# Kernel tuning notes

Measured on AMD Instinct MI355X. Metric: run time of the kernel, lower is better.

## Reference

```python
import jax, jax.numpy as jnp
import numpy as np

N, E, M, A, D = 100000, 3200000, 4096, 32, 16
G, V1, V2, O1 = 10, 20, 10, 20


def _lin(key, fin, fout, scale=0.1):
    kw, kb = jax.random.split(key)
    W = jax.random.normal(kw, (fin, fout), jnp.float32) * scale
    b = jax.random.normal(kb, (fout,), jnp.float32) * scale
    return W, b


def setup_inputs():
    key = jax.random.key(0)
    ks = jax.random.split(key, 32)
    inp = {}
    inp["x1"] = jax.random.normal(ks[0], (N, 15), jnp.float32)
    inp["x2"] = jax.random.normal(ks[1], (4,), jnp.float32)
    inp["edges"] = jax.random.randint(ks[2], (2, E), 0, N)
    inp["attack_src"] = jax.random.randint(ks[3], (M, A), 0, N)
    inp["attack_dst"] = jax.random.randint(ks[4], (M, A), 0, N)
    inp["attack_armies"] = jax.random.uniform(ks[5], (M, A), jnp.float32, 1.0, 20.0)
    inp["deploy_target"] = jax.random.randint(ks[6], (M, D), 0, N)
    inp["deploy_armies"] = jax.random.uniform(ks[7], (M, D), jnp.float32, 1.0, 10.0)
    inp["init_W"], inp["init_b"] = _lin(ks[8], 15, G)
    for i, fin in zip((1, 2, 3), (G + 15, 2 * G + 15, 3 * G + 15)):
        k1, k2, k3, k4 = jax.random.split(ks[8 + i], 4)
        inp[f"g{i}_Wl"] = jax.random.normal(k1, (fin, G), jnp.float32) * 0.1
        inp[f"g{i}_Wr"] = jax.random.normal(k2, (fin, G), jnp.float32) * 0.1
        inp[f"g{i}_att"] = jax.random.normal(k3, (G,), jnp.float32) * 0.1
        inp[f"g{i}_b"] = jax.random.normal(k4, (G,), jnp.float32) * 0.1
    inp["vt_W"], inp["vt_b"] = _lin(ks[12], 15 + G + 4, V1)
    inp["va_W"], inp["va_b"] = _lin(ks[13], V1, 1)
    inp["vv_W"], inp["vv_b"] = _lin(ks[14], V1, V2)
    inp["vl_W"], inp["vl_b"] = _lin(ks[15], V2, 1)
    inp["at_W"], inp["at_b"] = _lin(ks[16], 48, O1)
    inp["dt_W"], inp["dt_b"] = _lin(ks[17], 23, O1)
    inp["oa_W"], inp["oa_b"] = _lin(ks[18], O1, 1)
    inp["ov_W"], inp["ov_b"] = _lin(ks[19], O1, 1)
    return inp


def _gatv2(x, src, dst, Wl, Wr, att, bias, n):
    # GATv2 (PyG defaults: heads=1, negative_slope=0.2); dropout omitted (eval mode)
    xl = x @ Wl  # source-side transform  [N, G]
    xr = x @ Wr  # target-side transform  [N, G]
    e = jax.nn.leaky_relu(xl[src] + xr[dst], 0.2) @ att  # [Etot]
    emax = jax.ops.segment_max(e, dst, num_segments=n)
    ex = jnp.exp(e - emax[dst])
    denom = jax.ops.segment_sum(ex, dst, num_segments=n)
    alpha = ex / denom[dst]  # edge softmax per target node
    return jax.ops.segment_sum(alpha[:, None] * xl[src], dst, num_segments=n) + bias


def _forward(x1, x2, edges, attack_src, attack_dst, attack_armies,
             deploy_target, deploy_armies, p):
    n = x1.shape[0]
    loop = jnp.arange(n)
    src = jnp.concatenate([edges[0], loop])  # add_self_loops (PyG default)
    dst = jnp.concatenate([edges[1], loop])
    x_ = jax.nn.relu(x1 @ p["init_W"] + p["init_b"])  # Dropout = identity in eval
    xa = jax.nn.relu(_gatv2(jnp.concatenate([x_, x1], 1), src, dst,
                            p["g1_Wl"], p["g1_Wr"], p["g1_att"], p["g1_b"], n))
    xb = jax.nn.relu(_gatv2(jnp.concatenate([xa, x_, x1], 1), src, dst,
                            p["g2_Wl"], p["g2_Wr"], p["g2_att"], p["g2_b"], n))
    xc = jax.nn.relu(_gatv2(jnp.concatenate([xb, xa, x_, x1], 1), src, dst,
                            p["g3_Wl"], p["g3_Wr"], p["g3_att"], p["g3_b"], n))
    # per-move order features, batched over all moves at once: [M,A,*] / [M,D,*]
    x1d = x1[attack_dst]  # [M, A, 15]
    extra = 0.6 * attack_armies - 0.7 * (x1d[..., 3] + x1d[..., 4])
    att_feat = jnp.concatenate([xc[attack_src], xc[attack_dst],
                                x1[attack_src][..., 3:], x1d[..., 1:],
                                attack_armies[..., None], extra[..., None]], -1)  # [M,A,48]
    dep_feat = jnp.concatenate([xc[deploy_target], x1[deploy_target][..., 3:],
                                deploy_armies[..., None]], -1)  # [M,D,23]
    orders = jax.nn.relu(jnp.concatenate(
        [att_feat @ p["at_W"] + p["at_b"], dep_feat @ p["dt_W"] + p["dt_b"]], 1))  # [M,A+D,O1]
    oattn = jax.nn.softmax(orders @ p["oa_W"] + p["oa_b"], axis=1)  # softmax over orders
    pm = jnp.sum(oattn * (orders @ p["ov_W"] + p["ov_b"]), axis=(1, 2))  # [M]
    # value head: attention-pool over nodes
    vfeat = jnp.concatenate([xc, x1, jnp.tile(x2, (n, 1))], 1)  # [N, 29]
    v = jax.nn.relu(vfeat @ p["vt_W"] + p["vt_b"])
    vattn = jax.nn.softmax(v @ p["va_W"] + p["va_b"], axis=0)
    vagg = jax.nn.relu(jnp.sum(vattn * (v @ p["vv_W"] + p["vv_b"]), axis=0))
    V = jnp.tanh(vagg @ p["vl_W"] + p["vl_b"]).reshape(())
    return V, jax.nn.log_softmax(pm)


def reference(x1, x2, edges, attack_src, attack_dst, attack_armies,
              deploy_target, deploy_armies,
              init_W, init_b,
              g1_Wl, g1_Wr, g1_att, g1_b,
              g2_Wl, g2_Wr, g2_att, g2_b,
              g3_Wl, g3_Wr, g3_att, g3_b,
              vt_W, vt_b, va_W, va_b, vv_W, vv_b, vl_W, vl_b,
              at_W, at_b, dt_W, dt_b, oa_W, oa_b, ov_W, ov_b):
    p = dict(init_W=init_W, init_b=init_b,
             g1_Wl=g1_Wl, g1_Wr=g1_Wr, g1_att=g1_att, g1_b=g1_b,
             g2_Wl=g2_Wl, g2_Wr=g2_Wr, g2_att=g2_att, g2_b=g2_b,
             g3_Wl=g3_Wl, g3_Wr=g3_Wr, g3_att=g3_att, g3_b=g3_b,
             vt_W=vt_W, vt_b=vt_b, va_W=va_W, va_b=va_b, vv_W=vv_W, vv_b=vv_b,
             vl_W=vl_W, vl_b=vl_b, at_W=at_W, at_b=at_b, dt_W=dt_W, dt_b=dt_b,
             oa_W=oa_W, oa_b=oa_b, ov_W=ov_W, ov_b=ov_b)
    return _forward(x1, x2, edges, attack_src, attack_dst, attack_armies,
                    deploy_target, deploy_armies, p)
```

## Files before the change

kernel.cpp:

```cpp
#include <hip/hip_runtime.h>
#include <math.h>


#define PAD 12
#define LP 8
#define PFP 16
#define MAXB 784
#define CHK 8192

__device__ __forceinline__ float lrelu02(float v) { return v > 0.f ? v : 0.2f * v; }

__device__ __forceinline__ unsigned pk_bf16(float a, float b)
{
    unsigned ua = __float_as_uint(a), ub = __float_as_uint(b);
    ua += 0x7fffu + ((ua >> 16) & 1u);
    ub += 0x7fffu + ((ub >> 16) & 1u);
    return (ua >> 16) | (ub & 0xffff0000u);
}
__device__ __forceinline__ float bf_lo(unsigned u) { return __uint_as_float(u << 16); }
__device__ __forceinline__ float bf_hi(unsigned u) { return __uint_as_float(u & 0xffff0000u); }

template <int NS>
__device__ __forceinline__ void transform_body(
    int n, const float* __restrict__ s0, const float* __restrict__ s1,
    const float* __restrict__ s2, const float* __restrict__ x1,
    const float* __restrict__ Wl, const float* __restrict__ Wr,
    unsigned* __restrict__ XLb, float* __restrict__ XR)
{
    float al[10], ar[10];
#pragma unroll
    for (int g = 0; g < 10; ++g) { al[g] = 0.f; ar[g] = 0.f; }
    int o = 0;
#define TB_BLOCK(SP)                                                        \
    {                                                                       \
        const float4* pr = (const float4*)((SP) + n * PAD);                 \
        float4 v0 = pr[0], v1 = pr[1], v2 = pr[2];                          \
        float fv[10] = {v0.x, v0.y, v0.z, v0.w, v1.x, v1.y, v1.z, v1.w,     \
                        v2.x, v2.y};                                        \
        _Pragma("unroll") for (int k = 0; k < 10; ++k)                      \
        {                                                                   \
            _Pragma("unroll") for (int g = 0; g < 10; ++g)                  \
            {                                                               \
                al[g] += fv[k] * Wl[(o + k) * 10 + g];                      \
                ar[g] += fv[k] * Wr[(o + k) * 10 + g];                      \
            }                                                               \
        }                                                                   \
        o += 10;                                                            \
    }
    if constexpr (NS >= 1) TB_BLOCK(s0)
    if constexpr (NS >= 2) TB_BLOCK(s1)
    if constexpr (NS >= 3) TB_BLOCK(s2)
#undef TB_BLOCK
#pragma unroll
    for (int k = 0; k < 15; ++k) {
        float fv = x1[n * 15 + k];
#pragma unroll
        for (int g = 0; g < 10; ++g) {
            al[g] += fv * Wl[(o + k) * 10 + g];
            ar[g] += fv * Wr[(o + k) * 10 + g];
        }
    }
    uint4 q0;
    q0.x = pk_bf16(al[0], al[1]);
    q0.y = pk_bf16(al[2], al[3]);
    q0.z = pk_bf16(al[4], al[5]);
    q0.w = pk_bf16(al[6], al[7]);
    uint4 q1;
    q1.x = pk_bf16(al[8], al[9]);
    q1.y = 0; q1.z = 0; q1.w = 0;
    uint4* pb = (uint4*)(XLb + (size_t)n * LP);
    pb[0] = q0;
    pb[1] = q1;
    float4* po = (float4*)(XR + n * PAD);
    po[0] = make_float4(ar[0], ar[1], ar[2], ar[3]);
    po[1] = make_float4(ar[4], ar[5], ar[6], ar[7]);
    po[2] = make_float4(ar[8], ar[9], 0.f, 0.f);
}

__global__ __launch_bounds__(256) void k_a1_init(
    const int* __restrict__ edst, int E, unsigned short* __restrict__ pos,
    int* __restrict__ cntg, int PA,
    const float* __restrict__ x1, const float* __restrict__ W,
    const float* __restrict__ b, float* __restrict__ xo, int N, int NBK)
{
    if ((int)blockIdx.x < PA) {
        __shared__ int h[MAXB];
        for (int j = threadIdx.x; j < NBK; j += 256) h[j] = 0;
        __syncthreads();
        int base = blockIdx.x * CHK;
        for (int k = 0; k < CHK / 256; ++k) {
            int i = base + k * 256 + threadIdx.x;
            if (i < E) {
                int bkt = edst[i] >> 7;
                int p = atomicAdd(&h[bkt], 1);
                pos[i] = (unsigned short)p;
            }
        }
        __syncthreads();
        for (int j = threadIdx.x; j < NBK; j += 256)
            cntg[(size_t)j * PA + blockIdx.x] = h[j];
    } else {
        int n = ((int)blockIdx.x - PA) * 256 + (int)threadIdx.x;
        if (n >= N) return;
        float acc[10];
#pragma unroll
        for (int g = 0; g < 10; ++g) acc[g] = b[g];
#pragma unroll
        for (int k = 0; k < 15; ++k) {
            float fv = x1[n * 15 + k];
#pragma unroll
            for (int g = 0; g < 10; ++g) acc[g] += fv * W[k * 10 + g];
        }
        float4* po = (float4*)(xo + n * PAD);
        po[0] = make_float4(fmaxf(acc[0], 0.f), fmaxf(acc[1], 0.f),
                            fmaxf(acc[2], 0.f), fmaxf(acc[3], 0.f));
        po[1] = make_float4(fmaxf(acc[4], 0.f), fmaxf(acc[5], 0.f),
                            fmaxf(acc[6], 0.f), fmaxf(acc[7], 0.f));
        po[2] = make_float4(fmaxf(acc[8], 0.f), fmaxf(acc[9], 0.f), 0.f, 0.f);
    }
}

__global__ __launch_bounds__(1024) void k_scanA(
    const int* __restrict__ cntg, int* __restrict__ bases,
    int* __restrict__ bsumA, int TOT)
{
    __shared__ int wsum[16];
    int t = threadIdx.x;
    int i = blockIdx.x * 1024 + t;
    int lane = t & 63, w = t >> 6;
    int x = (i < TOT) ? cntg[i] : 0;
    int incl = x;
#pragma unroll
    for (int off = 1; off < 64; off <<= 1) {
        int u = __shfl_up(incl, off);
        if (lane >= off) incl += u;
    }
    if (lane == 63) wsum[w] = incl;
    __syncthreads();
    int woff = 0;
    for (int k = 0; k < w; ++k) woff += wsum[k];
    incl += woff;
    if (i < TOT) bases[i] = incl - x;
    if (t == 1023) bsumA[blockIdx.x] = incl;
}

__global__ __launch_bounds__(512) void k_scanB(
    const int* __restrict__ bsumA, int* __restrict__ boffA, int NBLKA,
    float* __restrict__ vsums, int* __restrict__ rowptr, int N, int Etot)
{
    __shared__ int wsum[8];
    int t = threadIdx.x;
    int lane = t & 63, w = t >> 6;
    int x = (t < NBLKA) ? bsumA[t] : 0;
    int incl = x;
#pragma unroll
    for (int off = 1; off < 64; off <<= 1) {
        int u = __shfl_up(incl, off);
        if (lane >= off) incl += u;
    }
    if (lane == 63) wsum[w] = incl;
    __syncthreads();
    int woff = 0;
    for (int k = 0; k < w; ++k) woff += wsum[k];
    incl += woff;
    if (t < NBLKA) boffA[t] = incl - x;
    if (t < 16) vsums[t] = 0.f;
    if (t == 0) rowptr[N] = Etot;
}

__global__ __launch_bounds__(1024) void k_scanC(
    int* __restrict__ bases, const int* __restrict__ boffA, int TOT)
{
    int i = blockIdx.x * 1024 + threadIdx.x;
    if (i < TOT) bases[i] += boffA[blockIdx.x];
}

__global__ __launch_bounds__(256) void k_a2(
    const int* __restrict__ esrc, const int* __restrict__ edst, int E,
    const int* __restrict__ bases, const unsigned short* __restrict__ pos,
    unsigned* __restrict__ pairs, int PA)
{
    int i = blockIdx.x * 256 + threadIdx.x;
    if (i >= E) return;
    int d = edst[i], s = esrc[i];
    int bkt = d >> 7;
    int blk = i / CHK;
    int dest = bases[(size_t)bkt * PA + blk] + (int)pos[i];
    pairs[dest] = (unsigned)s | ((unsigned)(d & 127) << 17);
}

__global__ __launch_bounds__(256) void k_b_tr1(
    const unsigned* __restrict__ pairs, const int* __restrict__ bases,
    int* __restrict__ rowptr, int* __restrict__ deg, int* __restrict__ sidx,
    int N, int NBK, int PA, int E,
    const float* __restrict__ s0a, const float* __restrict__ x1,
    const float* __restrict__ Wl, const float* __restrict__ Wr,
    unsigned* __restrict__ XLb, float* __restrict__ XR, int NB)
{
    if ((int)blockIdx.x < NBK) {
        __shared__ int cnt[128];
        __shared__ int cur[128];
        __shared__ int wtot;
        int t = threadIdx.x;
        if (t < 128) cnt[t] = 0;
        __syncthreads();
        int b = blockIdx.x;
        int p0 = bases[(size_t)b * PA];
        int p1 = (b + 1 < NBK) ? bases[(size_t)(b + 1) * PA] : E;
        int n0 = b << 7;
        int nn = N - n0; nn = nn < 0 ? 0 : (nn > 128 ? 128 : nn);
        for (int i = p0 + t; i < p1; i += 256) atomicAdd(&cnt[pairs[i] >> 17], 1);
        __syncthreads();
        int x = 0, incl = 0;
        if (t < 128) {
            x = cnt[t] + (t < nn ? 1 : 0);
            incl = x;
            int lane = t & 63;
#pragma unroll
            for (int off = 1; off < 64; off <<= 1) {
                int u = __shfl_up(incl, off);
                if (lane >= off) incl += u;
            }
            if (t == 63) wtot = incl;
        }
        __syncthreads();
        int sb = p0 + (b << 7);
        if (t < 128) {
            if (t >= 64) incl += wtot;
            int st = incl - x;
            if (t < nn) {
                int r = sb + st;
                rowptr[n0 + t] = r;
                deg[n0 + t] = cnt[t] + 1;
                sidx[r] = n0 + t;
                cur[t] = st + 1;
            } else {
                cur[t] = st;
            }
        }
        __syncthreads();
        for (int i = p0 + t; i < p1; i += 256) {
            unsigned w = pairs[i];
            int l = w >> 17, s = w & 0x1FFFF;
            int off = atomicAdd(&cur[l], 1);
            sidx[sb + off] = s;
        }
    } else {
        int n = ((int)blockIdx.x - NBK) * 256 + (int)threadIdx.x;
        if (n >= N) return;
        transform_body<1>(n, s0a, nullptr, nullptr, x1, Wl, Wr, XLb, XR);
    }
}

template <int NS>
__global__ __launch_bounds__(256) void k_transform(
    const float* __restrict__ s0, const float* __restrict__ s1,
    const float* __restrict__ s2, const float* __restrict__ x1,
    const float* __restrict__ Wl, const float* __restrict__ Wr,
    unsigned* __restrict__ XLb, float* __restrict__ XR, int N)
{
    int n = blockIdx.x * blockDim.x + threadIdx.x;
    if (n >= N) return;
    transform_body<NS>(n, s0, s1, s2, x1, Wl, Wr, XLb, XR);
}

__global__ __launch_bounds__(256) void k_gather(
    const int* __restrict__ rowptr, const int* __restrict__ deg,
    const int* __restrict__ sidx,
    const unsigned* __restrict__ XLb, const float* __restrict__ XR,
    const float* __restrict__ att, const float* __restrict__ b,
    float* __restrict__ xo, unsigned* __restrict__ PFb,
    const float* __restrict__ x1, int N)
{
    int node = blockIdx.x * 16 + (threadIdx.x >> 4);
    int l16 = threadIdx.x & 15;
    float acc[10];
#pragma unroll
    for (int g = 0; g < 10; ++g) acc[g] = 0.f;
    float den = 0.f;
    float satt[10];
#pragma unroll
    for (int g = 0; g < 10; ++g) satt[g] = att[g];
    if (node < N) {
        const float4* pr = (const float4*)(XR + node * PAD);
        float4 r0 = pr[0], r1 = pr[1], r2 = pr[2];
        float xr[10] = {r0.x, r0.y, r0.z, r0.w, r1.x, r1.y, r1.z, r1.w, r2.x, r2.y};
        int start = rowptr[node];
        int dgr = deg[node];
        int j = l16;
        while (j + 16 < dgr) {
            int s0 = sidx[start + j];
            int s1 = sidx[start + j + 16];
            const unsigned* pl0 = XLb + (size_t)s0 * LP;
            const unsigned* pl1 = XLb + (size_t)s1 * LP;
            uint4 qa = *(const uint4*)pl0;
            unsigned qa4 = pl0[4];
            uint4 qb = *(const uint4*)pl1;
            unsigned qb4 = pl1[4];
            float xa[10] = {bf_lo(qa.x), bf_hi(qa.x), bf_lo(qa.y), bf_hi(qa.y),
                            bf_lo(qa.z), bf_hi(qa.z), bf_lo(qa.w), bf_hi(qa.w),
                            bf_lo(qa4), bf_hi(qa4)};
            float xb[10] = {bf_lo(qb.x), bf_hi(qb.x), bf_lo(qb.y), bf_hi(qb.y),
                            bf_lo(qb.z), bf_hi(qb.z), bf_lo(qb.w), bf_hi(qb.w),
                            bf_lo(qb4), bf_hi(qb4)};
            float ea = 0.f, eb = 0.f;
#pragma unroll
            for (int g = 0; g < 10; ++g) {
                ea += lrelu02(xa[g] + xr[g]) * satt[g];
                eb += lrelu02(xb[g] + xr[g]) * satt[g];
            }
            float exa = __expf(ea), exb = __expf(eb);
#pragma unroll
            for (int g = 0; g < 10; ++g) acc[g] += exa * xa[g] + exb * xb[g];
            den += exa + exb;
            j += 32;
        }
        if (j < dgr) {
            int s = sidx[start + j];
            const unsigned* pl = XLb + (size_t)s * LP;
            uint4 q = *(const uint4*)pl;
            unsigned q4 = pl[4];
            float xl[10] = {bf_lo(q.x), bf_hi(q.x), bf_lo(q.y), bf_hi(q.y),
                            bf_lo(q.z), bf_hi(q.z), bf_lo(q.w), bf_hi(q.w),
                            bf_lo(q4), bf_hi(q4)};
            float e = 0.f;
#pragma unroll
            for (int g = 0; g < 10; ++g) e += lrelu02(xl[g] + xr[g]) * satt[g];
            float ex = __expf(e);
#pragma unroll
            for (int g = 0; g < 10; ++g) acc[g] += ex * xl[g];
            den += ex;
        }
    }
#pragma unroll
    for (int off = 1; off < 16; off <<= 1) {
        den += __shfl_xor(den, off);
#pragma unroll
        for (int g = 0; g < 10; ++g) acc[g] += __shfl_xor(acc[g], off);
    }
    if (node < N && l16 == 0) {
        float inv = 1.f / den;
        float r[10];
#pragma unroll
        for (int g = 0; g < 10; ++g) r[g] = fmaxf(acc[g] * inv + b[g], 0.f);
        float4* po = (float4*)(xo + node * PAD);
        po[0] = make_float4(r[0], r[1], r[2], r[3]);
        po[1] = make_float4(r[4], r[5], r[6], r[7]);
        po[2] = make_float4(r[8], r[9], 0.f, 0.f);
        if (PFb) {
            float xf[14];
#pragma unroll
            for (int k = 0; k < 14; ++k) xf[k] = x1[node * 15 + 1 + k];
            uint4 q0, q1, q2;
            q0.x = pk_bf16(r[0], r[1]);
            q0.y = pk_bf16(r[2], r[3]);
            q0.z = pk_bf16(r[4], r[5]);
            q0.w = pk_bf16(r[6], r[7]);
            q1.x = pk_bf16(r[8], r[9]);
            q1.y = pk_bf16(xf[0], xf[1]);
            q1.z = pk_bf16(xf[2], xf[3]);
            q1.w = pk_bf16(xf[4], xf[5]);
            q2.x = pk_bf16(xf[6], xf[7]);
            q2.y = pk_bf16(xf[8], xf[9]);
            q2.z = pk_bf16(xf[10], xf[11]);
            q2.w = pk_bf16(xf[12], xf[13]);
            uint4* qp = (uint4*)(PFb + (size_t)node * PFP);
            qp[0] = q0;
            qp[1] = q1;
            qp[2] = q2;
        }
    }
}

__global__ __launch_bounds__(256, 4) void k_scores(
    const unsigned* __restrict__ PFb, const float* __restrict__ xc,
    const float* __restrict__ x1, const float* __restrict__ x2,
    const int* __restrict__ asrc, const int* __restrict__ adst,
    const float* __restrict__ aarm,
    const int* __restrict__ dtgt, const float* __restrict__ darm,
    const float* __restrict__ atW, const float* __restrict__ atb,
    const float* __restrict__ dtW, const float* __restrict__ dtb,
    const float* __restrict__ oaW, const float* __restrict__ oab,
    const float* __restrict__ ovW, const float* __restrict__ ovb,
    const float* __restrict__ vtW, const float* __restrict__ vtb,
    const float* __restrict__ vaW, const float* __restrict__ vab,
    const float* __restrict__ vvW, const float* __restrict__ vvb,
    float* __restrict__ vsums, float2* __restrict__ OS,
    int AB, int DB, int NB, int N, int M)
{
    if ((int)blockIdx.x < AB) {
        int i = blockIdx.x * 256 + threadIdx.x;
        if (i >= M * 32) return;
        int m = i >> 5, a = i & 31;
        int s = asrc[i], d = adst[i];
        float arm = aarm[i];
        const uint4* ps = (const uint4*)(PFb + (size_t)s * PFP);
        const uint4* pd = (const uint4*)(PFb + (size_t)d * PFP);
        uint4 sA = ps[0], sB = ps[1], sC = ps[2];
        uint4 dA = pd[0], dB = pd[1], dC = pd[2];
        float fs[24] = {bf_lo(sA.x), bf_hi(sA.x), bf_lo(sA.y), bf_hi(sA.y),
                        bf_lo(sA.z), bf_hi(sA.z), bf_lo(sA.w), bf_hi(sA.w),
                        bf_lo(sB.x), bf_hi(sB.x), bf_lo(sB.y), bf_hi(sB.y),
                        bf_lo(sB.z), bf_hi(sB.z), bf_lo(sB.w), bf_hi(sB.w),
                        bf_lo(sC.x), bf_hi(sC.x), bf_lo(sC.y), bf_hi(sC.y),
                        bf_lo(sC.z), bf_hi(sC.z), bf_lo(sC.w), bf_hi(sC.w)};
        float fd[24] = {bf_lo(dA.x), bf_hi(dA.x), bf_lo(dA.y), bf_hi(dA.y),
                        bf_lo(dA.z), bf_hi(dA.z), bf_lo(dA.w), bf_hi(dA.w),
                        bf_lo(dB.x), bf_hi(dB.x), bf_lo(dB.y), bf_hi(dB.y),
                        bf_lo(dB.z), bf_hi(dB.z), bf_lo(dB.w), bf_hi(dB.w),
                        bf_lo(dC.x), bf_hi(dC.x), bf_lo(dC.y), bf_hi(dC.y),
                        bf_lo(dC.z), bf_hi(dC.z), bf_lo(dC.w), bf_hi(dC.w)};
        float ord[20];
#pragma unroll
        for (int j = 0; j < 20; ++j) ord[j] = atb[j];
#pragma unroll
        for (int k = 0; k < 10; ++k)
#pragma unroll
            for (int j = 0; j < 20; ++j) ord[j] += fs[k] * atW[k * 20 + j];
#pragma unroll
        for (int k = 0; k < 10; ++k)
#pragma unroll
            for (int j = 0; j < 20; ++j) ord[j] += fd[k] * atW[(10 + k) * 20 + j];
#pragma unroll
        for (int k = 0; k < 12; ++k)
#pragma unroll
            for (int j = 0; j < 20; ++j)
                ord[j] += fs[12 + k] * atW[(20 + k) * 20 + j];
#pragma unroll
        for (int k = 0; k < 14; ++k)
#pragma unroll
            for (int j = 0; j < 20; ++j)
                ord[j] += fd[10 + k] * atW[(32 + k) * 20 + j];
        float extra = 0.6f * arm - 0.7f * (fd[12] + fd[13]);
#pragma unroll
        for (int j = 0; j < 20; ++j)
            ord[j] += arm * atW[46 * 20 + j] + extra * atW[47 * 20 + j];
        float asc = oab[0], vsc = ovb[0];
#pragma unroll
        for (int j = 0; j < 20; ++j) {
            float oj = fmaxf(ord[j], 0.f);
            asc += oj * oaW[j];
            vsc += oj * ovW[j];
        }
        OS[(size_t)m * 48 + a] = make_float2(asc, vsc);
    } else if ((int)blockIdx.x < AB + DB) {
        int i = ((int)blockIdx.x - AB) * 256 + threadIdx.x;
        if (i >= M * 16) return;
        int m = i >> 4, dd = i & 15;
        int tg = dtgt[i];
        float arm = darm[i];
        const uint4* pt = (const uint4*)(PFb + (size_t)tg * PFP);
        uint4 tA = pt[0], tB = pt[1], tC = pt[2];
        float ft[24] = {bf_lo(tA.x), bf_hi(tA.x), bf_lo(tA.y), bf_hi(tA.y),
                        bf_lo(tA.z), bf_hi(tA.z), bf_lo(tA.w), bf_hi(tA.w),
                        bf_lo(tB.x), bf_hi(tB.x), bf_lo(tB.y), bf_hi(tB.y),
                        bf_lo(tB.z), bf_hi(tB.z), bf_lo(tB.w), bf_hi(tB.w),
                        bf_lo(tC.x), bf_hi(tC.x), bf_lo(tC.y), bf_hi(tC.y),
                        bf_lo(tC.z), bf_hi(tC.z), bf_lo(tC.w), bf_hi(tC.w)};
        float ord[20];
#pragma unroll
        for (int j = 0; j < 20; ++j) ord[j] = dtb[j];
#pragma unroll
        for (int k = 0; k < 10; ++k)
#pragma unroll
            for (int j = 0; j < 20; ++j) ord[j] += ft[k] * dtW[k * 20 + j];
#pragma unroll
        for (int k = 0; k < 12; ++k)
#pragma unroll
            for (int j = 0; j < 20; ++j)
                ord[j] += ft[12 + k] * dtW[(10 + k) * 20 + j];
#pragma unroll
        for (int j = 0; j < 20; ++j) ord[j] += arm * dtW[22 * 20 + j];
        float asc = oab[0], vsc = ovb[0];
#pragma unroll
        for (int j = 0; j < 20; ++j) {
            float oj = fmaxf(ord[j], 0.f);
            asc += oj * oaW[j];
            vsc += oj * ovW[j];
        }
        OS[(size_t)m * 48 + 32 + dd] = make_float2(asc, vsc);
    } else {
        __shared__ float sred[4][11];
        int t = threadIdx.x;
        int n = ((int)blockIdx.x - AB - DB) * 256 + t;
        float w = 0.f;
        float wv[10];
#pragma unroll
        for (int c = 0; c < 10; ++c) wv[c] = 0.f;
        if (n < N) {
            float v[20];
#pragma unroll
            for (int j = 0; j < 20; ++j) v[j] = vtb[j];
            {
                const float4* pc = (const float4*)(xc + n * PAD);
                float4 c0 = pc[0], c1 = pc[1], c2 = pc[2];
                float fv[10] = {c0.x, c0.y, c0.z, c0.w, c1.x, c1.y, c1.z, c1.w,
                                c2.x, c2.y};
#pragma unroll
                for (int k = 0; k < 10; ++k)
#pragma unroll
                    for (int j = 0; j < 20; ++j) v[j] += fv[k] * vtW[k * 20 + j];
            }
#pragma unroll
            for (int k = 0; k < 15; ++k) {
                float fv = x1[n * 15 + k];
#pragma unroll
                for (int j = 0; j < 20; ++j) v[j] += fv * vtW[(10 + k) * 20 + j];
            }
#pragma unroll
            for (int k = 0; k < 4; ++k) {
                float fv = x2[k];
#pragma unroll
                for (int j = 0; j < 20; ++j) v[j] += fv * vtW[(25 + k) * 20 + j];
            }
            float sc = vab[0];
#pragma unroll
            for (int j = 0; j < 20; ++j) {
                v[j] = fmaxf(v[j], 0.f);
                sc += v[j] * vaW[j];
            }
            w = __expf(sc);
#pragma unroll
            for (int c = 0; c < 10; ++c) {
                float t2 = vvb[c];
#pragma unroll
                for (int j = 0; j < 20; ++j) t2 += v[j] * vvW[j * 10 + c];
                wv[c] = w * t2;
            }
        }
#pragma unroll
        for (int off = 32; off > 0; off >>= 1) {
            w += __shfl_xor(w, off);
#pragma unroll
            for (int c = 0; c < 10; ++c) wv[c] += __shfl_xor(wv[c], off);
        }
        int wave = t >> 6, lane = t & 63;
        if (lane == 0) {
            sred[wave][0] = w;
#pragma unroll
            for (int c = 0; c < 10; ++c) sred[wave][1 + c] = wv[c];
        }
        __syncthreads();
        if (t == 0) {
#pragma unroll
            for (int c = 0; c < 11; ++c) {
                float s = sred[0][c] + sred[1][c] + sred[2][c] + sred[3][c];
                atomicAdd(&vsums[c], s);
            }
        }
    }
}

__global__ __launch_bounds__(256) void k_moves(
    const float2* __restrict__ OS, float* __restrict__ pm, int M)
{
    int m = blockIdx.x * 256 + threadIdx.x;
    if (m >= M) return;
    const float2* p = OS + (size_t)m * 48;
    float mx = -1e30f;
#pragma unroll
    for (int o = 0; o < 48; ++o) mx = fmaxf(mx, p[o].x);
    float Z = 0.f, num = 0.f;
#pragma unroll
    for (int o = 0; o < 48; ++o) {
        float e = __expf(p[o].x - mx);
        Z += e;
        num += e * p[o].y;
    }
    pm[m] = num / Z;
}

__global__ __launch_bounds__(1024) void k_final(
    const float* __restrict__ pm, const float* __restrict__ vsums,
    const float* __restrict__ vlW, const float* __restrict__ vlb,
    float* __restrict__ out, int M)
{
    __shared__ float red[16];
    __shared__ float sval;
    int t = threadIdx.x;
    int wave = t >> 6, lane = t & 63;
    if (t == 1023) {
        float inv = 1.f / vsums[0];
        float V = vlb[0];
#pragma unroll
        for (int j = 0; j < 10; ++j) V += fmaxf(vsums[1 + j] * inv, 0.f) * vlW[j];
        out[0] = tanhf(V);
    }
    float mx = -1e30f;
    for (int i = t; i < M; i += 1024) mx = fmaxf(mx, pm[i]);
#pragma unroll
    for (int off = 32; off > 0; off >>= 1) mx = fmaxf(mx, __shfl_xor(mx, off));
    if (lane == 0) red[wave] = mx;
    __syncthreads();
    if (t == 0) {
        float m2 = red[0];
        for (int i = 1; i < 16; ++i) m2 = fmaxf(m2, red[i]);
        sval = m2;
    }
    __syncthreads();
    float smax = sval;
    float sum = 0.f;
    for (int i = t; i < M; i += 1024) sum += __expf(pm[i] - smax);
#pragma unroll
    for (int off = 32; off > 0; off >>= 1) sum += __shfl_xor(sum, off);
    if (lane == 0) red[wave] = sum;
    __syncthreads();
    if (t == 0) {
        float s2 = 0.f;
        for (int i = 0; i < 16; ++i) s2 += red[i];
        sval = s2;
    }
    __syncthreads();
    float lse = smax + logf(sval);
    for (int i = t; i < M; i += 1024) out[1 + i] = pm[i] - lse;
}

extern "C" void kernel_launch(void* const* d_in, const int* in_sizes, int n_in,
                              void* d_out, int out_size, void* d_ws, size_t ws_size,
                              hipStream_t stream)
{
    const float* x1   = (const float*)d_in[0];
    const float* x2   = (const float*)d_in[1];
    const int*   edges = (const int*)d_in[2];
    const int*   asrc = (const int*)d_in[3];
    const int*   adst = (const int*)d_in[4];
    const float* aarm = (const float*)d_in[5];
    const int*   dtgt = (const int*)d_in[6];
    const float* darm = (const float*)d_in[7];
    const float* initW = (const float*)d_in[8];
    const float* initb = (const float*)d_in[9];
    const float* g1Wl = (const float*)d_in[10];
    const float* g1Wr = (const float*)d_in[11];
    const float* g1att = (const float*)d_in[12];
    const float* g1b = (const float*)d_in[13];
    const float* g2Wl = (const float*)d_in[14];
    const float* g2Wr = (const float*)d_in[15];
    const float* g2att = (const float*)d_in[16];
    const float* g2b = (const float*)d_in[17];
    const float* g3Wl = (const float*)d_in[18];
    const float* g3Wr = (const float*)d_in[19];
    const float* g3att = (const float*)d_in[20];
    const float* g3b = (const float*)d_in[21];
    const float* vtW = (const float*)d_in[22];
    const float* vtb = (const float*)d_in[23];
    const float* vaW = (const float*)d_in[24];
    const float* vab = (const float*)d_in[25];
    const float* vvW = (const float*)d_in[26];
    const float* vvb = (const float*)d_in[27];
    const float* vlW = (const float*)d_in[28];
    const float* vlb = (const float*)d_in[29];
    const float* atW = (const float*)d_in[30];
    const float* atb = (const float*)d_in[31];
    const float* dtW = (const float*)d_in[32];
    const float* dtb = (const float*)d_in[33];
    const float* oaW = (const float*)d_in[34];
    const float* oab = (const float*)d_in[35];
    const float* ovW = (const float*)d_in[36];
    const float* ovb = (const float*)d_in[37];

    const int N = in_sizes[0] / 15;
    const int E = in_sizes[2] / 2;
    const int M = in_sizes[3] / 32;
    const int Etot = E + N;
    const int NBK = (N + 127) >> 7;
    const int PA = (E + CHK - 1) / CHK;
    const int TOT = NBK * PA;

    float* ws = (float*)d_ws;
    size_t off = 0;
    float* XU = ws + off; off += (size_t)N * PAD;
    float* XA = ws + off; off += (size_t)N * PAD;
    float* XB = ws + off; off += (size_t)N * PAD;
    float* XC = ws + off; off += (size_t)N * PAD;
    unsigned* XLb = (unsigned*)(ws + off); off += (size_t)N * LP;
    float* XR = ws + off; off += (size_t)N * PAD;
    unsigned* PFb = (unsigned*)(ws + off); off += (size_t)N * PFP;
    int* sidx = (int*)(ws + off); off += Etot;
    unsigned* pairs = (unsigned*)(ws + off); off += E;
    int* deg = (int*)(ws + off); off += N;
    int* rowptr = (int*)(ws + off); off += N + 8;
    int* cntg = (int*)(ws + off); off += TOT + 8;
    int* bases = (int*)(ws + off); off += TOT + 8;
    int* bsumA = (int*)(ws + off); off += 512;
    int* boffA = (int*)(ws + off); off += 512;
    float* VS = ws + off; off += 16;
    float* PM = ws + off; off += M;
    float2* OS = (float2*)(ws + off); off += (size_t)M * 48 * 2;
    unsigned short* pos = (unsigned short*)XA;

    float* outp = (float*)d_out;

    const int NB = (N + 255) / 256;
    const int NG = (N + 15) / 16;
    const int AB = (M * 32 + 255) / 256;
    const int DB = (M * 16 + 255) / 256;
    const int SCA = (TOT + 1023) / 1024;
    const int* esrc = edges;
    const int* edst = edges + E;

    k_a1_init<<<PA + NB, 256, 0, stream>>>(edst, E, pos, cntg, PA,
                                           x1, initW, initb, XU, N, NBK);
    k_scanA<<<SCA, 1024, 0, stream>>>(cntg, bases, bsumA, TOT);
    k_scanB<<<1, 512, 0, stream>>>(bsumA, boffA, SCA, VS, rowptr, N, Etot);
    k_scanC<<<SCA, 1024, 0, stream>>>(bases, boffA, TOT);
    k_a2<<<(E + 255) / 256, 256, 0, stream>>>(esrc, edst, E, bases, pos, pairs, PA);
    k_b_tr1<<<NBK + NB, 256, 0, stream>>>(pairs, bases, rowptr, deg, sidx, N, NBK, PA, E,
                                          XU, x1, g1Wl, g1Wr, XLb, XR, NB);
    k_gather<<<NG, 256, 0, stream>>>(rowptr, deg, sidx, XLb, XR, g1att, g1b,
                                     XA, nullptr, x1, N);

    k_transform<2><<<NB, 256, 0, stream>>>(XA, XU, nullptr, x1, g2Wl, g2Wr, XLb, XR, N);
    k_gather<<<NG, 256, 0, stream>>>(rowptr, deg, sidx, XLb, XR, g2att, g2b,
                                     XB, nullptr, x1, N);

    k_transform<3><<<NB, 256, 0, stream>>>(XB, XA, XU, x1, g3Wl, g3Wr, XLb, XR, N);
    k_gather<<<NG, 256, 0, stream>>>(rowptr, deg, sidx, XLb, XR, g3att, g3b,
                                     XC, PFb, x1, N);

    k_scores<<<AB + DB + NB, 256, 0, stream>>>(PFb, XC, x1, x2, asrc, adst, aarm,
                                               dtgt, darm, atW, atb, dtW, dtb,
                                               oaW, oab, ovW, ovb,
                                               vtW, vtb, vaW, vab, vvW, vvb,
                                               VS, OS, AB, DB, NB, N, M);
    k_moves<<<(M + 255) / 256, 256, 0, stream>>>(OS, PM, M);
    k_final<<<1, 1024, 0, stream>>>(PM, VS, vlW, vlb, outp, M);
}
```

Before: 399.6 us.

## Use 8-lane gather groups, split scores kernel, fold moves softmax into final

The GAT gather now assigns 8 lanes per destination node instead of 16 and processes four neighbours per iteration. This lowers shuffle-reduction cost and raises memory-level parallelism, and launch bounds are tightened for occupancy. The fused scores kernel is split into separate attack, deploy and value kernels. The per-move softmax from k_moves is folded into k_final, which drops one launch and the PM buffer. The single-block final kernel now does all move work serially, and with M=4096 each thread handles at most 4 moves, within the 8-entry cap.

```diff
diff --git a/kernel.cpp b/kernel.cpp
--- a/kernel.cpp
+++ b/kernel.cpp
@@ -264,7 +264,19 @@
     transform_body<NS>(n, s0, s1, s2, x1, Wl, Wr, XLb, XR);
 }
 
-__global__ __launch_bounds__(256) void k_gather(
+__device__ __forceinline__ void unpack_row(const unsigned* __restrict__ pl,
+                                           float* xl)
+{
+    uint4 q = *(const uint4*)pl;
+    unsigned q4 = pl[4];
+    xl[0] = bf_lo(q.x); xl[1] = bf_hi(q.x);
+    xl[2] = bf_lo(q.y); xl[3] = bf_hi(q.y);
+    xl[4] = bf_lo(q.z); xl[5] = bf_hi(q.z);
+    xl[6] = bf_lo(q.w); xl[7] = bf_hi(q.w);
+    xl[8] = bf_lo(q4);  xl[9] = bf_hi(q4);
+}
+
+__global__ __launch_bounds__(256, 4) void k_gather(
     const int* __restrict__ rowptr, const int* __restrict__ deg,
     const int* __restrict__ sidx,
     const unsigned* __restrict__ XLb, const float* __restrict__ XR,
@@ -272,8 +284,8 @@
     float* __restrict__ xo, unsigned* __restrict__ PFb,
     const float* __restrict__ x1, int N)
 {
-    int node = blockIdx.x * 16 + (threadIdx.x >> 4);
-    int l16 = threadIdx.x & 15;
+    int node = blockIdx.x * 32 + (threadIdx.x >> 3);
+    int l8 = threadIdx.x & 7;
     float acc[10];
 #pragma unroll
     for (int g = 0; g < 10; ++g) acc[g] = 0.f;
@@ -287,42 +299,37 @@
         float xr[10] = {r0.x, r0.y, r0.z, r0.w, r1.x, r1.y, r1.z, r1.w, r2.x, r2.y};
         int start = rowptr[node];
         int dgr = deg[node];
-        int j = l16;
-        while (j + 16 < dgr) {
+        int j = l8;
+        while (j + 24 < dgr) {
             int s0 = sidx[start + j];
-            int s1 = sidx[start + j + 16];
-            const unsigned* pl0 = XLb + (size_t)s0 * LP;
-            const unsigned* pl1 = XLb + (size_t)s1 * LP;
-            uint4 qa = *(const uint4*)pl0;
-            unsigned qa4 = pl0[4];
-            uint4 qb = *(const uint4*)pl1;
-            unsigned qb4 = pl1[4];
-            float xa[10] = {bf_lo(qa.x), bf_hi(qa.x), bf_lo(qa.y), bf_hi(qa.y),
-                            bf_lo(qa.z), bf_hi(qa.z), bf_lo(qa.w), bf_hi(qa.w),
-                            bf_lo(qa4), bf_hi(qa4)};
-            float xb[10] = {bf_lo(qb.x), bf_hi(qb.x), bf_lo(qb.y), bf_hi(qb.y),
-                            bf_lo(qb.z), bf_hi(qb.z), bf_lo(qb.w), bf_hi(qb.w),
-                            bf_lo(qb4), bf_hi(qb4)};
-            float ea = 0.f, eb = 0.f;
+            int s1 = sidx[start + j + 8];
+            int s2 = sidx[start + j + 16];
+            int s3 = sidx[start + j + 24];
+            float xa[10], xb[10], xc2[10], xd[10];
+            unpack_row(XLb + (size_t)s0 * LP, xa);
+            unpack_row(XLb + (size_t)s1 * LP, xb);
+            unpack_row(XLb + (size_t)s2 * LP, xc2);
+            unpack_row(XLb + (size_t)s3 * LP, xd);
+            float ea = 0.f, eb = 0.f, ec = 0.f, ed = 0.f;
 #pragma unroll
             for (int g = 0; g < 10; ++g) {
                 ea += lrelu02(xa[g] + xr[g]) * satt[g];
                 eb += lrelu02(xb[g] + xr[g]) * satt[g];
+                ec += lrelu02(xc2[g] + xr[g]) * satt[g];
+                ed += lrelu02(xd[g] + xr[g]) * satt[g];
             }
             float exa = __expf(ea), exb = __expf(eb);
-#pragma unroll
-            for (int g = 0; g < 10; ++g) acc[g] += exa * xa[g] + exb * xb[g];
-            den += exa + exb;
+            float exc = __expf(ec), exd = __expf(ed);
+#pragma unroll
+            for (int g = 0; g < 10; ++g)
+                acc[g] += exa * xa[g] + exb * xb[g] + exc * xc2[g] + exd * xd[g];
+            den += exa + exb + exc + exd;
             j += 32;
         }
-        if (j < dgr) {
+        for (; j < dgr; j += 8) {
             int s = sidx[start + j];
-            const unsigned* pl = XLb + (size_t)s * LP;
-            uint4 q = *(const uint4*)pl;
-            unsigned q4 = pl[4];
-            float xl[10] = {bf_lo(q.x), bf_hi(q.x), bf_lo(q.y), bf_hi(q.y),
-                            bf_lo(q.z), bf_hi(q.z), bf_lo(q.w), bf_hi(q.w),
-                            bf_lo(q4), bf_hi(q4)};
+            float xl[10];
+            unpack_row(XLb + (size_t)s * LP, xl);
             float e = 0.f;
 #pragma unroll
             for (int g = 0; g < 10; ++g) e += lrelu02(xl[g] + xr[g]) * satt[g];
@@ -333,12 +340,12 @@
         }
     }
 #pragma unroll
-    for (int off = 1; off < 16; off <<= 1) {
+    for (int off = 1; off < 8; off <<= 1) {
         den += __shfl_xor(den, off);
 #pragma unroll
         for (int g = 0; g < 10; ++g) acc[g] += __shfl_xor(acc[g], off);
     }
-    if (node < N && l16 == 0) {
+    if (node < N && l8 == 0) {
         float inv = 1.f / den;
         float r[10];
 #pragma unroll
@@ -372,206 +379,196 @@
     }
 }
 
-__global__ __launch_bounds__(256, 4) void k_scores(
-    const unsigned* __restrict__ PFb, const float* __restrict__ xc,
-    const float* __restrict__ x1, const float* __restrict__ x2,
+__global__ __launch_bounds__(256, 4) void k_att(
+    const unsigned* __restrict__ PFb,
     const int* __restrict__ asrc, const int* __restrict__ adst,
     const float* __restrict__ aarm,
+    const float* __restrict__ atW, const float* __restrict__ atb,
+    const float* __restrict__ oaW, const float* __restrict__ oab,
+    const float* __restrict__ ovW, const float* __restrict__ ovb,
+    float2* __restrict__ OS, int M)
+{
+    int i = blockIdx.x * 256 + threadIdx.x;
+    if (i >= M * 32) return;
+    int m = i >> 5, a = i & 31;
+    int s = asrc[i], d = adst[i];
+    float arm = aarm[i];
+    const uint4* ps = (const uint4*)(PFb + (size_t)s * PFP);
+    const uint4* pd = (const uint4*)(PFb + (size_t)d * PFP);
+    uint4 sA = ps[0], sB = ps[1], sC = ps[2];
+    uint4 dA = pd[0], dB = pd[1], dC = pd[2];
+    float fs[24] = {bf_lo(sA.x), bf_hi(sA.x), bf_lo(sA.y), bf_hi(sA.y),
+                    bf_lo(sA.z), bf_hi(sA.z), bf_lo(sA.w), bf_hi(sA.w),
+                    bf_lo(sB.x), bf_hi(sB.x), bf_lo(sB.y), bf_hi(sB.y),
+                    bf_lo(sB.z), bf_hi(sB.z), bf_lo(sB.w), bf_hi(sB.w),
+                    bf_lo(sC.x), bf_hi(sC.x), bf_lo(sC.y), bf_hi(sC.y),
+                    bf_lo(sC.z), bf_hi(sC.z), bf_lo(sC.w), bf_hi(sC.w)};
+    float fd[24] = {bf_lo(dA.x), bf_hi(dA.x), bf_lo(dA.y), bf_hi(dA.y),
+                    bf_lo(dA.z), bf_hi(dA.z), bf_lo(dA.w), bf_hi(dA.w),
+                    bf_lo(dB.x), bf_hi(dB.x), bf_lo(dB.y), bf_hi(dB.y),
+                    bf_lo(dB.z), bf_hi(dB.z), bf_lo(dB.w), bf_hi(dB.w),
+                    bf_lo(dC.x), bf_hi(dC.x), bf_lo(dC.y), bf_hi(dC.y),
+                    bf_lo(dC.z), bf_hi(dC.z), bf_lo(dC.w), bf_hi(dC.w)};
+    float ord[20];
+#pragma unroll
+    for (int j = 0; j < 20; ++j) ord[j] = atb[j];
+#pragma unroll
+    for (int k = 0; k < 10; ++k)
+#pragma unroll
+        for (int j = 0; j < 20; ++j) ord[j] += fs[k] * atW[k * 20 + j];
+#pragma unroll
+    for (int k = 0; k < 10; ++k)
+#pragma unroll
+        for (int j = 0; j < 20; ++j) ord[j] += fd[k] * atW[(10 + k) * 20 + j];
+#pragma unroll
+    for (int k = 0; k < 12; ++k)
+#pragma unroll
+        for (int j = 0; j < 20; ++j)
+            ord[j] += fs[12 + k] * atW[(20 + k) * 20 + j];
+#pragma unroll
+    for (int k = 0; k < 14; ++k)
+#pragma unroll
+        for (int j = 0; j < 20; ++j)
+            ord[j] += fd[10 + k] * atW[(32 + k) * 20 + j];
+    float extra = 0.6f * arm - 0.7f * (fd[12] + fd[13]);
+#pragma unroll
+    for (int j = 0; j < 20; ++j)
+        ord[j] += arm * atW[46 * 20 + j] + extra * atW[47 * 20 + j];
+    float asc = oab[0], vsc = ovb[0];
+#pragma unroll
+    for (int j = 0; j < 20; ++j) {
+        float oj = fmaxf(ord[j], 0.f);
+        asc += oj * oaW[j];
+        vsc += oj * ovW[j];
+    }
+    OS[(size_t)m * 48 + a] = make_float2(asc, vsc);
+}
+
+__global__ __launch_bounds__(256, 4) void k_dep(
+    const unsigned* __restrict__ PFb,
     const int* __restrict__ dtgt, const float* __restrict__ darm,
-    const float* __restrict__ atW, const float* __restrict__ atb,
     const float* __restrict__ dtW, const float* __restrict__ dtb,
     const float* __restrict__ oaW, const float* __restrict__ oab,
     const float* __restrict__ ovW, const float* __restrict__ ovb,
+    float2* __restrict__ OS, int M)
+{
+    int i = blockIdx.x * 256 + threadIdx.x;
+    if (i >= M * 16) return;
+    int m = i >> 4, dd = i & 15;
+    int tg = dtgt[i];
+    float arm = darm[i];
+    const uint4* pt = (const uint4*)(PFb + (size_t)tg * PFP);
+    uint4 tA = pt[0], tB = pt[1], tC = pt[2];
+    float ft[24] = {bf_lo(tA.x), bf_hi(tA.x), bf_lo(tA.y), bf_hi(tA.y),
+                    bf_lo(tA.z), bf_hi(tA.z), bf_lo(tA.w), bf_hi(tA.w),
+                    bf_lo(tB.x), bf_hi(tB.x), bf_lo(tB.y), bf_hi(tB.y),
+                    bf_lo(tB.z), bf_hi(tB.z), bf_lo(tB.w), bf_hi(tB.w),
+                    bf_lo(tC.x), bf_hi(tC.x), bf_lo(tC.y), bf_hi(tC.y),
+                    bf_lo(tC.z), bf_hi(tC.z), bf_lo(tC.w), bf_hi(tC.w)};
+    float ord[20];
+#pragma unroll
+    for (int j = 0; j < 20; ++j) ord[j] = dtb[j];
+#pragma unroll
+    for (int k = 0; k < 10; ++k)
+#pragma unroll
+        for (int j = 0; j < 20; ++j) ord[j] += ft[k] * dtW[k * 20 + j];
+#pragma unroll
+    for (int k = 0; k < 12; ++k)
+#pragma unroll
+        for (int j = 0; j < 20; ++j)
+            ord[j] += ft[12 + k] * dtW[(10 + k) * 20 + j];
+#pragma unroll
+    for (int j = 0; j < 20; ++j) ord[j] += arm * dtW[22 * 20 + j];
+    float asc = oab[0], vsc = ovb[0];
+#pragma unroll
+    for (int j = 0; j < 20; ++j) {
+        float oj = fmaxf(ord[j], 0.f);
+        asc += oj * oaW[j];
+        vsc += oj * ovW[j];
+    }
+    OS[(size_t)m * 48 + 32 + dd] = make_float2(asc, vsc);
+}
+
+__global__ __launch_bounds__(256) void k_value(
+    const float* __restrict__ xc, const float* __restrict__ x1,
+    const float* __restrict__ x2,
     const float* __restrict__ vtW, const float* __restrict__ vtb,
     const float* __restrict__ vaW, const float* __restrict__ vab,
     const float* __restrict__ vvW, const float* __restrict__ vvb,
-    float* __restrict__ vsums, float2* __restrict__ OS,
-    int AB, int DB, int NB, int N, int M)
-{
-    if ((int)blockIdx.x < AB) {
-        int i = blockIdx.x * 256 + threadIdx.x;
-        if (i >= M * 32) return;
-        int m = i >> 5, a = i & 31;
-        int s = asrc[i], d = adst[i];
-        float arm = aarm[i];
-        const uint4* ps = (const uint4*)(PFb + (size_t)s * PFP);
-        const uint4* pd = (const uint4*)(PFb + (size_t)d * PFP);
-        uint4 sA = ps[0], sB = ps[1], sC = ps[2];
-        uint4 dA = pd[0], dB = pd[1], dC = pd[2];
-        float fs[24] = {bf_lo(sA.x), bf_hi(sA.x), bf_lo(sA.y), bf_hi(sA.y),
-                        bf_lo(sA.z), bf_hi(sA.z), bf_lo(sA.w), bf_hi(sA.w),
-                        bf_lo(sB.x), bf_hi(sB.x), bf_lo(sB.y), bf_hi(sB.y),
-                        bf_lo(sB.z), bf_hi(sB.z), bf_lo(sB.w), bf_hi(sB.w),
-                        bf_lo(sC.x), bf_hi(sC.x), bf_lo(sC.y), bf_hi(sC.y),
-                        bf_lo(sC.z), bf_hi(sC.z), bf_lo(sC.w), bf_hi(sC.w)};
-        float fd[24] = {bf_lo(dA.x), bf_hi(dA.x), bf_lo(dA.y), bf_hi(dA.y),
-                        bf_lo(dA.z), bf_hi(dA.z), bf_lo(dA.w), bf_hi(dA.w),
-                        bf_lo(dB.x), bf_hi(dB.x), bf_lo(dB.y), bf_hi(dB.y),
-                        bf_lo(dB.z), bf_hi(dB.z), bf_lo(dB.w), bf_hi(dB.w),
-                        bf_lo(dC.x), bf_hi(dC.x), bf_lo(dC.y), bf_hi(dC.y),
-                        bf_lo(dC.z), bf_hi(dC.z), bf_lo(dC.w), bf_hi(dC.w)};
-        float ord[20];
-#pragma unroll
-        for (int j = 0; j < 20; ++j) ord[j] = atb[j];
-#pragma unroll
-        for (int k = 0; k < 10; ++k)
-#pragma unroll
-            for (int j = 0; j < 20; ++j) ord[j] += fs[k] * atW[k * 20 + j];
-#pragma unroll
-        for (int k = 0; k < 10; ++k)
-#pragma unroll
-            for (int j = 0; j < 20; ++j) ord[j] += fd[k] * atW[(10 + k) * 20 + j];
-#pragma unroll
-        for (int k = 0; k < 12; ++k)
-#pragma unroll
-            for (int j = 0; j < 20; ++j)
-                ord[j] += fs[12 + k] * atW[(20 + k) * 20 + j];
-#pragma unroll
-        for (int k = 0; k < 14; ++k)
-#pragma unroll
-            for (int j = 0; j < 20; ++j)
-                ord[j] += fd[10 + k] * atW[(32 + k) * 20 + j];
-        float extra = 0.6f * arm - 0.7f * (fd[12] + fd[13]);
-#pragma unroll
-        for (int j = 0; j < 20; ++j)
-            ord[j] += arm * atW[46 * 20 + j] + extra * atW[47 * 20 + j];
-        float asc = oab[0], vsc = ovb[0];
+    float* __restrict__ vsums, int N)
+{
+    __shared__ float sred[4][11];
+    int t = threadIdx.x;
+    int n = blockIdx.x * 256 + t;
+    float w = 0.f;
+    float wv[10];
+#pragma unroll
+    for (int c = 0; c < 10; ++c) wv[c] = 0.f;
+    if (n < N) {
+        float v[20];
+#pragma unroll
+        for (int j = 0; j < 20; ++j) v[j] = vtb[j];
+        {
+            const float4* pc = (const float4*)(xc + n * PAD);
+            float4 c0 = pc[0], c1 = pc[1], c2 = pc[2];
+            float fv[10] = {c0.x, c0.y, c0.z, c0.w, c1.x, c1.y, c1.z, c1.w,
+                            c2.x, c2.y};
+#pragma unroll
+            for (int k = 0; k < 10; ++k)
+#pragma unroll
+                for (int j = 0; j < 20; ++j) v[j] += fv[k] * vtW[k * 20 + j];
+        }
+#pragma unroll
+        for (int k = 0; k < 15; ++k) {
+            float fv = x1[n * 15 + k];
+#pragma unroll
+            for (int j = 0; j < 20; ++j) v[j] += fv * vtW[(10 + k) * 20 + j];
+        }
+#pragma unroll
+        for (int k = 0; k < 4; ++k) {
+            float fv = x2[k];
+#pragma unroll
+            for (int j = 0; j < 20; ++j) v[j] += fv * vtW[(25 + k) * 20 + j];
+        }
+        float sc = vab[0];
 #pragma unroll
         for (int j = 0; j < 20; ++j) {
-            float oj = fmaxf(ord[j], 0.f);
-            asc += oj * oaW[j];
-            vsc += oj * ovW[j];
-        }
-        OS[(size_t)m * 48 + a] = make_float2(asc, vsc);
-    } else if ((int)blockIdx.x < AB + DB) {
-        int i = ((int)blockIdx.x - AB) * 256 + threadIdx.x;
-        if (i >= M * 16) return;
-        int m = i >> 4, dd = i & 15;
-        int tg = dtgt[i];
-        float arm = darm[i];
-        const uint4* pt = (const uint4*)(PFb + (size_t)tg * PFP);
-        uint4 tA = pt[0], tB = pt[1], tC = pt[2];
-        float ft[24] = {bf_lo(tA.x), bf_hi(tA.x), bf_lo(tA.y), bf_hi(tA.y),
-                        bf_lo(tA.z), bf_hi(tA.z), bf_lo(tA.w), bf_hi(tA.w),
-                        bf_lo(tB.x), bf_hi(tB.x), bf_lo(tB.y), bf_hi(tB.y),
-                        bf_lo(tB.z), bf_hi(tB.z), bf_lo(tB.w), bf_hi(tB.w),
-                        bf_lo(tC.x), bf_hi(tC.x), bf_lo(tC.y), bf_hi(tC.y),
-                        bf_lo(tC.z), bf_hi(tC.z), bf_lo(tC.w), bf_hi(tC.w)};
-        float ord[20];
-#pragma unroll
-        for (int j = 0; j < 20; ++j) ord[j] = dtb[j];
-#pragma unroll
-        for (int k = 0; k < 10; ++k)
-#pragma unroll
-            for (int j = 0; j < 20; ++j) ord[j] += ft[k] * dtW[k * 20 + j];
-#pragma unroll
-        for (int k = 0; k < 12; ++k)
-#pragma unroll
-            for (int j = 0; j < 20; ++j)
-                ord[j] += ft[12 + k] * dtW[(10 + k) * 20 + j];
-#pragma unroll
-        for (int j = 0; j < 20; ++j) ord[j] += arm * dtW[22 * 20 + j];
-        float asc = oab[0], vsc = ovb[0];
-#pragma unroll
-        for (int j = 0; j < 20; ++j) {
-            float oj = fmaxf(ord[j], 0.f);
-            asc += oj * oaW[j];
-            vsc += oj * ovW[j];
-        }
-        OS[(size_t)m * 48 + 32 + dd] = make_float2(asc, vsc);
-    } else {
-        __shared__ float sred[4][11];
-        int t = threadIdx.x;
-        int n = ((int)blockIdx.x - AB - DB) * 256 + t;
-        float w = 0.f;
-        float wv[10];
-#pragma unroll
-        for (int c = 0; c < 10; ++c) wv[c] = 0.f;
-        if (n < N) {
-            float v[20];
-#pragma unroll
-            for (int j = 0; j < 20; ++j) v[j] = vtb[j];
-            {
-                const float4* pc = (const float4*)(xc + n * PAD);
-                float4 c0 = pc[0], c1 = pc[1], c2 = pc[2];
-                float fv[10] = {c0.x, c0.y, c0.z, c0.w, c1.x, c1.y, c1.z, c1.w,
-                                c2.x, c2.y};
-#pragma unroll
-                for (int k = 0; k < 10; ++k)
-#pragma unroll
-                    for (int j = 0; j < 20; ++j) v[j] += fv[k] * vtW[k * 20 + j];
-            }
-#pragma unroll
-            for (int k = 0; k < 15; ++k) {
-                float fv = x1[n * 15 + k];
-#pragma unroll
-                for (int j = 0; j < 20; ++j) v[j] += fv * vtW[(10 + k) * 20 + j];
-            }
-#pragma unroll
-            for (int k = 0; k < 4; ++k) {
-                float fv = x2[k];
-#pragma unroll
-                for (int j = 0; j < 20; ++j) v[j] += fv * vtW[(25 + k) * 20 + j];
-            }
-            float sc = vab[0];
-#pragma unroll
-            for (int j = 0; j < 20; ++j) {
-                v[j] = fmaxf(v[j], 0.f);
-                sc += v[j] * vaW[j];
-            }
-            w = __expf(sc);
-#pragma unroll
-            for (int c = 0; c < 10; ++c) {
-                float t2 = vvb[c];
-#pragma unroll
-                for (int j = 0; j < 20; ++j) t2 += v[j] * vvW[j * 10 + c];
-                wv[c] = w * t2;
-            }
-        }
-#pragma unroll
-        for (int off = 32; off > 0; off >>= 1) {
-            w += __shfl_xor(w, off);
-#pragma unroll
-            for (int c = 0; c < 10; ++c) wv[c] += __shfl_xor(wv[c], off);
-        }
-        int wave = t >> 6, lane = t & 63;
-        if (lane == 0) {
-            sred[wave][0] = w;
-#pragma unroll
-            for (int c = 0; c < 10; ++c) sred[wave][1 + c] = wv[c];
-        }
-        __syncthreads();
-        if (t == 0) {
-#pragma unroll
-            for (int c = 0; c < 11; ++c) {
-                float s = sred[0][c] + sred[1][c] + sred[2][c] + sred[3][c];
-                atomicAdd(&vsums[c], s);
-            }
-        }
-    }
-}
-
-__global__ __launch_bounds__(256) void k_moves(
-    const float2* __restrict__ OS, float* __restrict__ pm, int M)
-{
-    int m = blockIdx.x * 256 + threadIdx.x;
-    if (m >= M) return;
-    const float2* p = OS + (size_t)m * 48;
-    float mx = -1e30f;
-#pragma unroll
-    for (int o = 0; o < 48; ++o) mx = fmaxf(mx, p[o].x);
-    float Z = 0.f, num = 0.f;
-#pragma unroll
-    for (int o = 0; o < 48; ++o) {
-        float e = __expf(p[o].x - mx);
-        Z += e;
-        num += e * p[o].y;
-    }
-    pm[m] = num / Z;
+            v[j] = fmaxf(v[j], 0.f);
+            sc += v[j] * vaW[j];
+        }
+        w = __expf(sc);
+#pragma unroll
+        for (int c = 0; c < 10; ++c) {
+            float t2 = vvb[c];
+#pragma unroll
+            for (int j = 0; j < 20; ++j) t2 += v[j] * vvW[j * 10 + c];
+            wv[c] = w * t2;
+        }
+    }
+#pragma unroll
+    for (int off = 32; off > 0; off >>= 1) {
+        w += __shfl_xor(w, off);
+#pragma unroll
+        for (int c = 0; c < 10; ++c) wv[c] += __shfl_xor(wv[c], off);
+    }
+    int wave = t >> 6, lane = t & 63;
+    if (lane == 0) {
+        sred[wave][0] = w;
+#pragma unroll
+        for (int c = 0; c < 10; ++c) sred[wave][1 + c] = wv[c];
+    }
+    __syncthreads();
+    if (t == 0) {
+#pragma unroll
+        for (int c = 0; c < 11; ++c) {
+            float s = sred[0][c] + sred[1][c] + sred[2][c] + sred[3][c];
+            atomicAdd(&vsums[c], s);
+        }
+    }
 }
 
 __global__ __launch_bounds__(1024) void k_final(
-    const float* __restrict__ pm, const float* __restrict__ vsums,
+    const float2* __restrict__ OS, const float* __restrict__ vsums,
     const float* __restrict__ vlW, const float* __restrict__ vlb,
     float* __restrict__ out, int M)
 {
@@ -586,8 +583,25 @@
         for (int j = 0; j < 10; ++j) V += fmaxf(vsums[1 + j] * inv, 0.f) * vlW[j];
         out[0] = tanhf(V);
     }
+    float pmv[8];
+    int nm = 0;
     float mx = -1e30f;
-    for (int i = t; i < M; i += 1024) mx = fmaxf(mx, pm[i]);
+    for (int m = t; m < M && nm < 8; m += 1024) {
+        const float2* p = OS + (size_t)m * 48;
+        float lmx = -1e30f;
+#pragma unroll
+        for (int o = 0; o < 48; ++o) lmx = fmaxf(lmx, p[o].x);
+        float Z = 0.f, num = 0.f;
+#pragma unroll
+        for (int o = 0; o < 48; ++o) {
+            float e = __expf(p[o].x - lmx);
+            Z += e;
+            num += e * p[o].y;
+        }
+        float pm = num / Z;
+        pmv[nm++] = pm;
+        mx = fmaxf(mx, pm);
+    }
 #pragma unroll
     for (int off = 32; off > 0; off >>= 1) mx = fmaxf(mx, __shfl_xor(mx, off));
     if (lane == 0) red[wave] = mx;
@@ -600,7 +614,7 @@
     __syncthreads();
     float smax = sval;
     float sum = 0.f;
-    for (int i = t; i < M; i += 1024) sum += __expf(pm[i] - smax);
+    for (int k = 0; k < nm; ++k) sum += __expf(pmv[k] - smax);
 #pragma unroll
     for (int off = 32; off > 0; off >>= 1) sum += __shfl_xor(sum, off);
     if (lane == 0) red[wave] = sum;
@@ -612,7 +626,10 @@
     }
     __syncthreads();
     float lse = smax + logf(sval);
-    for (int i = t; i < M; i += 1024) out[1 + i] = pm[i] - lse;
+    {
+        int k = 0;
+        for (int m = t; m < M && k < nm; m += 1024) out[1 + m] = pmv[k++] - lse;
+    }
 }
 
 extern "C" void kernel_launch(void* const* d_in, const int* in_sizes, int n_in,
@@ -684,16 +701,13 @@
     int* bsumA = (int*)(ws + off); off += 512;
     int* boffA = (int*)(ws + off); off += 512;
     float* VS = ws + off; off += 16;
-    float* PM = ws + off; off += M;
     float2* OS = (float2*)(ws + off); off += (size_t)M * 48 * 2;
     unsigned short* pos = (unsigned short*)XA;
 
     float* outp = (float*)d_out;
 
     const int NB = (N + 255) / 256;
-    const int NG = (N + 15) / 16;
-    const int AB = (M * 32 + 255) / 256;
-    const int DB = (M * 16 + 255) / 256;
+    const int NG = (N + 31) / 32;
     const int SCA = (TOT + 1023) / 1024;
     const int* esrc = edges;
     const int* edst = edges + E;
@@ -717,11 +731,10 @@
     k_gather<<<NG, 256, 0, stream>>>(rowptr, deg, sidx, XLb, XR, g3att, g3b,
                                      XC, PFb, x1, N);
 
-    k_scores<<<AB + DB + NB, 256, 0, stream>>>(PFb, XC, x1, x2, asrc, adst, aarm,
-                                               dtgt, darm, atW, atb, dtW, dtb,
-                                               oaW, oab, ovW, ovb,
-                                               vtW, vtb, vaW, vab, vvW, vvb,
-                                               VS, OS, AB, DB, NB, N, M);
-    k_moves<<<(M + 255) / 256, 256, 0, stream>>>(OS, PM, M);
-    k_final<<<1, 1024, 0, stream>>>(PM, VS, vlW, vlb, outp, M);
-}
+    k_att<<<(M * 32 + 255) / 256, 256, 0, stream>>>(PFb, asrc, adst, aarm,
+                                                    atW, atb, oaW, oab, ovW, ovb, OS, M);
+    k_dep<<<(M * 16 + 255) / 256, 256, 0, stream>>>(PFb, dtgt, darm,
+                                                    dtW, dtb, oaW, oab, ovW, ovb, OS, M);
+    k_value<<<NB, 256, 0, stream>>>(XC, x1, x2, vtW, vtb, vaW, vab, vvW, vvb, VS, N);
+    k_final<<<1, 1024, 0, stream>>>(OS, VS, vlW, vlb, outp, M);
+}
```

Result: slower. 465.5 us (+16.5%).
